# Optimization experiments

Measured on AMD Instinct MI355X. Metric: run time of the kernel, lower is better.

## Reference

```python
import jax, jax.numpy as jnp
import numpy as np

N = 100_000   # nodes
E = 1_000_000 # edges
D_IN = 64
H = 64
G = 64        # graphs in batch
OUT = 2


def gcn_conv(x, edge_index, W, b):
    # PyG GCNConv: add self-loops, symmetric D^-1/2 (A+I) D^-1/2 normalization
    h = x @ W                                   # [N, H]
    src, dst = edge_index[0], edge_index[1]
    n = x.shape[0]
    deg = jax.ops.segment_sum(jnp.ones(E, x.dtype), dst, num_segments=n) + 1.0  # +1 self loop
    dinv = jax.lax.rsqrt(deg)                   # [N]
    norm = dinv[src] * dinv[dst]                # [E]
    msg = h[src] * norm[:, None]                # gather + scale [E, H]
    agg = jax.ops.segment_sum(msg, dst, num_segments=n)
    agg = agg + h * (dinv * dinv)[:, None]      # self-loop term
    return agg + b


def setup_inputs() -> dict:
    key = jax.random.key(0)
    ks = jax.random.split(key, 8)
    x = jax.random.normal(ks[0], (N, D_IN), jnp.float32)
    edge_index = jax.random.randint(ks[1], (2, E), 0, N, dtype=jnp.int64)
    batch = jnp.sort(jax.random.randint(ks[2], (N,), 0, G, dtype=jnp.int64))
    graph_feats = jax.random.normal(ks[3], (G, 1), jnp.float32)
    W1 = jax.random.normal(ks[4], (D_IN, H), jnp.float32) / np.sqrt(D_IN)
    b1 = jnp.zeros((H,), jnp.float32)
    W2 = jax.random.normal(ks[5], (H, H), jnp.float32) / np.sqrt(H)
    b2 = jnp.zeros((H,), jnp.float32)
    Wlin = jax.random.normal(ks[6], (H + 1, OUT), jnp.float32) / np.sqrt(H + 1)
    blin = jnp.zeros((OUT,), jnp.float32)
    return {"x": x, "edge_index": edge_index, "batch": batch,
            "graph_feats": graph_feats, "W1": W1, "b1": b1,
            "W2": W2, "b2": b2, "Wlin": Wlin, "blin": blin}


def reference(x, edge_index, batch, graph_feats, W1, b1, W2, b2, Wlin, blin):
    h = jax.nn.relu(gcn_conv(x, edge_index, W1, b1))
    # dropout is identity in eval mode
    h = jax.nn.relu(gcn_conv(h, edge_index, W2, b2))
    pooled = jax.ops.segment_sum(h, batch, num_segments=G)  # global_add_pool [G, H]
    feats = jnp.concatenate([pooled, graph_feats], axis=1)  # [G, H+1]
    return feats @ Wlin + blin
```

## Files before the change

### kernel.cpp

```cpp
#include <hip/hip_runtime.h>

#define H 64
#define G 64
#define OUT 2
#define MAXBUK 128
#define BSHIFT 10
#define CAP 12288

typedef unsigned int uint32;
using short8 = __attribute__((ext_vector_type(8))) short;
using f32x4  = __attribute__((ext_vector_type(4))) float;

union ABFrag { uint32 u[4]; uint4 q; short8 v; };

__device__ inline float bf16lo(uint32 u) { return __uint_as_float(u << 16); }
__device__ inline float bf16hi(uint32 u) { return __uint_as_float(u & 0xffff0000u); }
__device__ inline uint32 packbf16(float a, float b) {
    uint32 ua = __float_as_uint(a);
    uint32 ub = __float_as_uint(b);
    ua = (ua + 0x7fffu + ((ua >> 16) & 1u)) >> 16;
    ub = (ub + 0x7fffu + ((ub >> 16) & 1u)) & 0xffff0000u;
    return ua | ub;
}

__global__ __launch_bounds__(256) void k_setup(const float* __restrict__ W1,
                                               const float* __restrict__ W2,
                                               uint32* __restrict__ Wb,
                                               float* __restrict__ pooled,
                                               int* __restrict__ bcnt) {
    int blk = blockIdx.x;
    int t = threadIdx.x;
    if (blk < 2) {
        const float* W = blk ? W2 : W1;
        uint32* dw = Wb + blk * 2048;
        for (int i = t; i < 2048; i += 256) {
            int r = i & 3;
            int lane = (i >> 2) & 63;
            int slot = i >> 8;
            int ct = slot >> 1, ks = slot & 1;
            int col = ct * 16 + (lane & 15);
            int k0 = ks * 32 + (lane >> 4) * 8;
            float a = W[(k0 + 2 * r) * 64 + col];
            float b = W[(k0 + 2 * r + 1) * 64 + col];
            dw[i] = packbf16(a, b);
        }
    } else {
        for (int i = t; i < G * H; i += 256) pooled[i] = 0.0f;
        if (t < MAXBUK) bcnt[t] = 0;
    }
}

__global__ __launch_bounds__(256) void k_bhist(const int* __restrict__ dst,
                                               int* __restrict__ bcnt, int e, int nbuk) {
    __shared__ int h[MAXBUK];
    for (int i = threadIdx.x; i < MAXBUK; i += 256) h[i] = 0;
    __syncthreads();
    int stride = gridDim.x * 256;
    for (int i = blockIdx.x * 256 + threadIdx.x; i < e; i += stride)
        atomicAdd(&h[__builtin_nontemporal_load(&dst[i]) >> BSHIFT], 1);
    __syncthreads();
    for (int i = threadIdx.x; i < nbuk; i += 256)
        if (h[i]) atomicAdd(&bcnt[i], h[i]);
}

__global__ void k_bscan(const int* __restrict__ bcnt, int* __restrict__ bbase,
                        int* __restrict__ bcur, int nbuk) {
    if (threadIdx.x == 0) {
        int run = 0;
        for (int i = 0; i < nbuk; ++i) {
            bbase[i] = run; bcur[i] = run; run += bcnt[i];
        }
        bbase[nbuk] = run;
    }
}

__global__ __launch_bounds__(256) void k_bscatter(const int* __restrict__ src,
                                                  const int* __restrict__ dst,
                                                  int* __restrict__ bcur,
                                                  int2* __restrict__ inter, int e) {
    __shared__ int cnt[MAXBUK];
    __shared__ int run[MAXBUK];
    int per = (e + gridDim.x - 1) / gridDim.x;
    int lo = blockIdx.x * per, hi = min(lo + per, e);
    for (int i = threadIdx.x; i < MAXBUK; i += 256) cnt[i] = 0;
    __syncthreads();
    for (int i = lo + threadIdx.x; i < hi; i += 256)
        atomicAdd(&cnt[dst[i] >> BSHIFT], 1);
    __syncthreads();
    if (threadIdx.x < MAXBUK) {
        int c = cnt[threadIdx.x];
        run[threadIdx.x] = c ? atomicAdd(&bcur[threadIdx.x], c) : 0;
        cnt[threadIdx.x] = 0;
    }
    __syncthreads();
    for (int i = lo + threadIdx.x; i < hi; i += 256) {
        int d = dst[i];
        int s = src[i];
        int b = d >> BSHIFT;
        int pos = run[b] + atomicAdd(&cnt[b], 1);
        inter[pos] = make_int2(s, d);
    }
}

__global__ __launch_bounds__(256) void k_build(const int2* __restrict__ inter,
                                               const int* __restrict__ bbase,
                                               int* __restrict__ rowptr,
                                               float* __restrict__ dinv,
                                               int* __restrict__ csr,
                                               int n, int nbuk) {
    __shared__ int cnt[1024];
    __shared__ int scn[1024];
    __shared__ int part[256];
    __shared__ int stage[CAP];
    int b = blockIdx.x;
    int t = threadIdx.x;
    int nlo = b << BSHIFT;
    int nhi = min(nlo + 1024, n);
    int nn = nhi - nlo;
    int e0 = bbase[b], e1 = bbase[b + 1];
    int ne = e1 - e0;
    for (int i = t; i < nn; i += 256) cnt[i] = 0;
    __syncthreads();
    for (int i = t; i < ne; i += 256)
        atomicAdd(&cnt[inter[e0 + i].y - nlo], 1);
    __syncthreads();
    int base4 = 4 * t;
    int sum = 0;
    for (int j = 0; j < 4; ++j) {
        int idx = base4 + j;
        int v = (idx < nn) ? cnt[idx] : 0;
        if (idx < nn) scn[idx] = sum;
        sum += v;
    }
    part[t] = sum;
    __syncthreads();
    for (int off = 1; off < 256; off <<= 1) {
        int v = (t >= off) ? part[t - off] : 0;
        __syncthreads();
        part[t] += v;
        __syncthreads();
    }
    int pbase = (t == 0) ? 0 : part[t - 1];
    for (int j = 0; j < 4; ++j) {
        int idx = base4 + j;
        if (idx < nn) scn[idx] += pbase;
    }
    __syncthreads();
    for (int i = t; i < nn; i += 256) {
        rowptr[nlo + i] = e0 + scn[i];
        dinv[nlo + i] = rsqrtf((float)cnt[i] + 1.0f);
    }
    if (b == 0 && t == 0) rowptr[n] = bbase[nbuk];
    for (int i = t; i < nn; i += 256) cnt[i] = 0;
    __syncthreads();
    for (int i = t; i < ne; i += 256) {
        int2 p = inter[e0 + i];
        int ln = p.y - nlo;
        int pos = scn[ln] + atomicAdd(&cnt[ln], 1);
        if (pos < CAP) stage[pos] = p.x;
        else csr[e0 + pos] = p.x;
    }
    __syncthreads();
    int m = min(ne, CAP);
    for (int i = t; i < m; i += 256) csr[e0 + i] = stage[i];
}

template <int BFIN>
__global__ __launch_bounds__(256) void k_gemm_mfma(const void* __restrict__ Xv,
                                                   const uint32* __restrict__ Wb,
                                                   const float* __restrict__ dinv,
                                                   uint32* __restrict__ Y, int n) {
    int lane = threadIdx.x & 63;
    int wave = threadIdx.x >> 6;
    int l15 = lane & 15;
    int grp = lane >> 4;
    ABFrag bf[4][2];
    const uint4* Wb4 = (const uint4*)Wb;
#pragma unroll
    for (int ct = 0; ct < 4; ++ct)
#pragma unroll
        for (int ks = 0; ks < 2; ++ks)
            bf[ct][ks].q = Wb4[(ct * 2 + ks) * 64 + lane];

    int rbase0 = blockIdx.x * 128 + wave * 32;
    f32x4 acc[2][4] = {};
#pragma unroll
    for (int sub = 0; sub < 2; ++sub) {
        int row = min(rbase0 + sub * 16 + l15, n - 1);
        ABFrag a[2];
        if (BFIN) {
            const uint4* X4 = (const uint4*)Xv;
#pragma unroll
            for (int ks = 0; ks < 2; ++ks)
                a[ks].q = X4[(size_t)row * 8 + ks * 4 + grp];
        } else {
            const float4* X4 = (const float4*)Xv;
#pragma unroll
            for (int ks = 0; ks < 2; ++ks) {
                float4 f0 = X4[(size_t)row * 16 + ks * 8 + grp * 2];
                float4 f1 = X4[(size_t)row * 16 + ks * 8 + grp * 2 + 1];
                a[ks].u[0] = packbf16(f0.x, f0.y);
                a[ks].u[1] = packbf16(f0.z, f0.w);
                a[ks].u[2] = packbf16(f1.x, f1.y);
                a[ks].u[3] = packbf16(f1.z, f1.w);
            }
        }
#pragma unroll
        for (int ct = 0; ct < 4; ++ct) {
            acc[sub][ct] = __builtin_amdgcn_mfma_f32_16x16x32_bf16(a[0].v, bf[ct][0].v,
                                                                   acc[sub][ct], 0, 0, 0);
            acc[sub][ct] = __builtin_amdgcn_mfma_f32_16x16x32_bf16(a[1].v, bf[ct][1].v,
                                                                   acc[sub][ct], 0, 0, 0);
        }
    }
#pragma unroll
    for (int sub = 0; sub < 2; ++sub) {
        int rb = rbase0 + sub * 16;
#pragma unroll
        for (int r = 0; r < 4; ++r) {
            int row = rb + grp * 4 + r;
            float dd = dinv[min(row, n - 1)];
#pragma unroll
            for (int ct = 0; ct < 4; ++ct) {
                float v = acc[sub][ct][r] * dd;
                float w = __shfl_xor(v, 1);
                if (!(lane & 1) && row < n)
                    Y[(size_t)row * 32 + ct * 8 + (l15 >> 1)] = packbf16(v, w);
            }
        }
    }
}

template <int DOPOOL>
__global__ __launch_bounds__(256) void k_aggregate(const uint32* __restrict__ h,
                                                   const int* __restrict__ csrs,
                                                   const int* __restrict__ rowptr,
                                                   const float* __restrict__ dinv,
                                                   const float* __restrict__ b,
                                                   const int* __restrict__ batch,
                                                   uint32* __restrict__ hout,
                                                   float* __restrict__ pooled, int n) {
    __shared__ float red[8][64];
    __shared__ int sg[8];
    int tid = threadIdx.x;
    int wave = tid >> 6;
    int lane = tid & 63;
    int half = lane >> 5;
    int hl = lane & 31;
    int slot = wave * 2 + half;
    int node = blockIdx.x * 8 + slot;
    bool active = node < n;
    float o0 = 0.f, o1 = 0.f;
    if (active) {
        int r0 = rowptr[node];
        int r1 = rowptr[node + 1];
        int m = r1 - 1;
        int mc = max(m, 0);
        uint32 sv = h[(size_t)node * 32 + hl];
        float acc0 = bf16lo(sv);
        float acc1 = bf16hi(sv);
        int s[16];
#pragma unroll
        for (int j = 0; j < 16; ++j)
            s[j] = __builtin_nontemporal_load(&csrs[min(r0 + j, mc)]);
        uint32 g[16];
#pragma unroll
        for (int j = 0; j < 16; ++j)
            g[j] = (r0 + j <= m) ? h[(size_t)s[j] * 32 + hl] : 0u;
#pragma unroll
        for (int j = 0; j < 16; ++j) {
            acc0 += bf16lo(g[j]);
            acc1 += bf16hi(g[j]);
        }
        for (int e = r0 + 16; e < r1; e += 8) {
            int t1 = min(e + 1, m), t2 = min(e + 2, m), t3 = min(e + 3, m);
            int t4 = min(e + 4, m), t5 = min(e + 5, m), t6 = min(e + 6, m);
            int t7 = min(e + 7, m);
            int u0 = csrs[e],  u1 = csrs[t1], u2 = csrs[t2], u3 = csrs[t3];
            int u4 = csrs[t4], u5 = csrs[t5], u6 = csrs[t6], u7 = csrs[t7];
            uint32 q0 = h[(size_t)u0 * 32 + hl];
            uint32 q1 = (e + 1 <= m) ? h[(size_t)u1 * 32 + hl] : 0u;
            uint32 q2 = (e + 2 <= m) ? h[(size_t)u2 * 32 + hl] : 0u;
            uint32 q3 = (e + 3 <= m) ? h[(size_t)u3 * 32 + hl] : 0u;
            uint32 q4 = (e + 4 <= m) ? h[(size_t)u4 * 32 + hl] : 0u;
            uint32 q5 = (e + 5 <= m) ? h[(size_t)u5 * 32 + hl] : 0u;
            uint32 q6 = (e + 6 <= m) ? h[(size_t)u6 * 32 + hl] : 0u;
            uint32 q7 = (e + 7 <= m) ? h[(size_t)u7 * 32 + hl] : 0u;
            acc0 += (bf16lo(q0) + bf16lo(q1)) + (bf16lo(q2) + bf16lo(q3)) +
                    (bf16lo(q4) + bf16lo(q5)) + (bf16lo(q6) + bf16lo(q7));
            acc1 += (bf16hi(q0) + bf16hi(q1)) + (bf16hi(q2) + bf16hi(q3)) +
                    (bf16hi(q4) + bf16hi(q5)) + (bf16hi(q6) + bf16hi(q7));
        }
        float dd = dinv[node];
        o0 = acc0 * dd + b[2 * hl + 0];
        o1 = acc1 * dd + b[2 * hl + 1];
        o0 = o0 > 0.f ? o0 : 0.f;
        o1 = o1 > 0.f ? o1 : 0.f;
        if (!DOPOOL) hout[(size_t)node * 32 + hl] = packbf16(o0, o1);
    }
    if (DOPOOL) {
        red[slot][2 * hl + 0] = active ? o0 : 0.f;
        red[slot][2 * hl + 1] = active ? o1 : 0.f;
        if (hl == 0) sg[slot] = active ? batch[node] : -1;
        __syncthreads();
        if (wave == 0) {
            float s = red[0][lane];
            int gcur = sg[0];
            for (int w = 1; w < 8; ++w) {
                int gw = sg[w];
                if (gw < 0) break;
                if (gw == gcur) {
                    s += red[w][lane];
                } else {
                    if (gcur >= 0) atomicAdd(&pooled[gcur * H + lane], s);
                    s = red[w][lane];
                    gcur = gw;
                }
            }
            if (gcur >= 0) atomicAdd(&pooled[gcur * H + lane], s);
        }
    }
}

__global__ void k_final(const float* __restrict__ pooled, const float* __restrict__ gf,
                        const float* __restrict__ Wlin, const float* __restrict__ blin,
                        float* __restrict__ out) {
    int t = threadIdx.x;
    if (t >= G * OUT) return;
    int g = t >> 1, o = t & 1;
    float acc = blin[o];
#pragma unroll
    for (int j = 0; j < 64; ++j) acc += pooled[g * H + j] * Wlin[j * OUT + o];
    acc += gf[g] * Wlin[64 * OUT + o];
    out[g * OUT + o] = acc;
}

extern "C" void kernel_launch(void* const* d_in, const int* in_sizes, int n_in,
                              void* d_out, int out_size, void* d_ws, size_t ws_size,
                              hipStream_t stream) {
    const float* x          = (const float*)d_in[0];
    const int*   edge_index = (const int*)d_in[1];
    const int*   batch      = (const int*)d_in[2];
    const float* gf         = (const float*)d_in[3];
    const float* W1         = (const float*)d_in[4];
    const float* b1         = (const float*)d_in[5];
    const float* W2         = (const float*)d_in[6];
    const float* b2         = (const float*)d_in[7];
    const float* Wlin       = (const float*)d_in[8];
    const float* blin       = (const float*)d_in[9];
    float* out = (float*)d_out;

    const int N = in_sizes[0] / H;
    const int E = in_sizes[1] / 2;
    const int* src = edge_index;
    const int* dst = edge_index + E;
    const int NBUK = (N + (1 << BSHIFT) - 1) >> BSHIFT;

    float* ws = (float*)d_ws;
    float* dinv   = ws;
    uint32* bufA  = (uint32*)(dinv + N);
    uint32* bufB  = bufA + (size_t)N * 32;
    float* pooled = (float*)(bufB + (size_t)N * 32);
    int*   rowptr = (int*)(pooled + G * H);
    int*   bcnt   = rowptr + (N + 1);
    int*   bbase  = bcnt + MAXBUK;
    int*   bcur   = bbase + (MAXBUK + 1);
    size_t off = (size_t)(bcur + MAXBUK - (int*)d_ws);
    off = (off + 3) & ~(size_t)3;
    uint32* Wb   = (uint32*)d_ws + off;
    int*   csrs  = (int*)(Wb + 2 * 2048);
    size_t off2 = (size_t)(csrs + E - (int*)d_ws);
    off2 = (off2 + 1) & ~(size_t)1;
    int2*  inter = (int2*)((int*)d_ws + off2);

    const int T = 256;

    k_setup<<<3, T, 0, stream>>>(W1, W2, Wb, pooled, bcnt);
    k_bhist<<<256, T, 0, stream>>>(dst, bcnt, E, NBUK);
    k_bscan<<<1, 64, 0, stream>>>(bcnt, bbase, bcur, NBUK);
    k_bscatter<<<128, T, 0, stream>>>(src, dst, bcur, inter, E);
    k_build<<<NBUK, T, 0, stream>>>(inter, bbase, rowptr, dinv, csrs, N, NBUK);

    const int NBG = (N + 127) / 128;

    k_gemm_mfma<0><<<NBG, T, 0, stream>>>(x, Wb, dinv, bufA, N);
    k_aggregate<0><<<(N + 7) / 8, T, 0, stream>>>(bufA, csrs, rowptr, dinv, b1, batch,
                                                  bufB, pooled, N);

    k_gemm_mfma<1><<<NBG, T, 0, stream>>>(bufB, Wb + 2048, dinv, bufA, N);
    k_aggregate<1><<<(N + 7) / 8, T, 0, stream>>>(bufA, csrs, rowptr, dinv, b2, batch,
                                                  nullptr, pooled, N);

    k_final<<<1, 128, 0, stream>>>(pooled, gf, Wlin, blin, out);
}
```

Baseline: 175.6 us.

## Fold bucket scan into histogram, pack edge records, vectorize aggregation gathers

```diff
diff --git a/kernel.cpp b/kernel.cpp
--- a/kernel.cpp
+++ b/kernel.cpp
@@ -27,7 +27,8 @@
                                                const float* __restrict__ W2,
                                                uint32* __restrict__ Wb,
                                                float* __restrict__ pooled,
-                                               int* __restrict__ bcnt) {
+                                               int* __restrict__ bcnt,
+                                               int* __restrict__ done) {
     int blk = blockIdx.x;
     int t = threadIdx.x;
     if (blk < 2) {
@@ -47,37 +48,43 @@
     } else {
         for (int i = t; i < G * H; i += 256) pooled[i] = 0.0f;
         if (t < MAXBUK) bcnt[t] = 0;
+        if (t == 0) *done = 0;
     }
 }
 
 __global__ __launch_bounds__(256) void k_bhist(const int* __restrict__ dst,
-                                               int* __restrict__ bcnt, int e, int nbuk) {
-    __shared__ int h[MAXBUK];
-    for (int i = threadIdx.x; i < MAXBUK; i += 256) h[i] = 0;
+                                               int* __restrict__ bcnt,
+                                               int* __restrict__ bbase,
+                                               int* __restrict__ bcur,
+                                               int* __restrict__ done,
+                                               int e, int nbuk) {
+    __shared__ int hh[MAXBUK];
+    for (int i = threadIdx.x; i < MAXBUK; i += 256) hh[i] = 0;
     __syncthreads();
     int stride = gridDim.x * 256;
     for (int i = blockIdx.x * 256 + threadIdx.x; i < e; i += stride)
-        atomicAdd(&h[__builtin_nontemporal_load(&dst[i]) >> BSHIFT], 1);
+        atomicAdd(&hh[__builtin_nontemporal_load(&dst[i]) >> BSHIFT], 1);
     __syncthreads();
     for (int i = threadIdx.x; i < nbuk; i += 256)
-        if (h[i]) atomicAdd(&bcnt[i], h[i]);
-}
-
-__global__ void k_bscan(const int* __restrict__ bcnt, int* __restrict__ bbase,
-                        int* __restrict__ bcur, int nbuk) {
+        if (hh[i]) atomicAdd(&bcnt[i], hh[i]);
     if (threadIdx.x == 0) {
-        int run = 0;
-        for (int i = 0; i < nbuk; ++i) {
-            bbase[i] = run; bcur[i] = run; run += bcnt[i];
-        }
-        bbase[nbuk] = run;
+        __threadfence();
+        int ticket = atomicAdd(done, 1);
+        if (ticket == (int)gridDim.x - 1) {
+            int run = 0;
+            for (int i = 0; i < nbuk; ++i) {
+                int c = atomicAdd(&bcnt[i], 0);
+                bbase[i] = run; bcur[i] = run; run += c;
+            }
+            bbase[nbuk] = run;
+        }
     }
 }
 
 __global__ __launch_bounds__(256) void k_bscatter(const int* __restrict__ src,
                                                   const int* __restrict__ dst,
                                                   int* __restrict__ bcur,
-                                                  int2* __restrict__ inter, int e) {
+                                                  uint32* __restrict__ inter, int e) {
     __shared__ int cnt[MAXBUK];
     __shared__ int run[MAXBUK];
     int per = (e + gridDim.x - 1) / gridDim.x;
@@ -97,12 +104,13 @@
         int d = dst[i];
         int s = src[i];
         int b = d >> BSHIFT;
+        int ln = d & ((1 << BSHIFT) - 1);
         int pos = run[b] + atomicAdd(&cnt[b], 1);
-        inter[pos] = make_int2(s, d);
-    }
-}
-
-__global__ __launch_bounds__(256) void k_build(const int2* __restrict__ inter,
+        inter[pos] = ((uint32)ln << 17) | (uint32)s;
+    }
+}
+
+__global__ __launch_bounds__(256) void k_build(const uint32* __restrict__ inter,
                                                const int* __restrict__ bbase,
                                                int* __restrict__ rowptr,
                                                float* __restrict__ dinv,
@@ -122,7 +130,7 @@
     for (int i = t; i < nn; i += 256) cnt[i] = 0;
     __syncthreads();
     for (int i = t; i < ne; i += 256)
-        atomicAdd(&cnt[inter[e0 + i].y - nlo], 1);
+        atomicAdd(&cnt[inter[e0 + i] >> 17], 1);
     __syncthreads();
     int base4 = 4 * t;
     int sum = 0;
@@ -154,11 +162,12 @@
     for (int i = t; i < nn; i += 256) cnt[i] = 0;
     __syncthreads();
     for (int i = t; i < ne; i += 256) {
-        int2 p = inter[e0 + i];
-        int ln = p.y - nlo;
+        uint32 p = inter[e0 + i];
+        int ln = p >> 17;
+        int s = p & 0x1FFFF;
         int pos = scn[ln] + atomicAdd(&cnt[ln], 1);
-        if (pos < CAP) stage[pos] = p.x;
-        else csr[e0 + pos] = p.x;
+        if (pos < CAP) stage[pos] = s;
+        else csr[e0 + pos] = s;
     }
     __syncthreads();
     int m = min(ne, CAP);
@@ -247,60 +256,79 @@
     int lane = tid & 63;
     int half = lane >> 5;
     int hl = lane & 31;
+    int grp = hl >> 3;
+    int sub = hl & 7;
     int slot = wave * 2 + half;
     int node = blockIdx.x * 8 + slot;
     bool active = node < n;
-    float o0 = 0.f, o1 = 0.f;
+    const uint4* h4 = (const uint4*)h;
+    float acc[8] = {};
+    float o[8] = {};
     if (active) {
         int r0 = rowptr[node];
         int r1 = rowptr[node + 1];
         int m = r1 - 1;
-        int mc = max(m, 0);
-        uint32 sv = h[(size_t)node * 32 + hl];
-        float acc0 = bf16lo(sv);
-        float acc1 = bf16hi(sv);
-        int s[16];
-#pragma unroll
-        for (int j = 0; j < 16; ++j)
-            s[j] = __builtin_nontemporal_load(&csrs[min(r0 + j, mc)]);
-        uint32 g[16];
-#pragma unroll
-        for (int j = 0; j < 16; ++j)
-            g[j] = (r0 + j <= m) ? h[(size_t)s[j] * 32 + hl] : 0u;
-#pragma unroll
-        for (int j = 0; j < 16; ++j) {
-            acc0 += bf16lo(g[j]);
-            acc1 += bf16hi(g[j]);
-        }
-        for (int e = r0 + 16; e < r1; e += 8) {
-            int t1 = min(e + 1, m), t2 = min(e + 2, m), t3 = min(e + 3, m);
-            int t4 = min(e + 4, m), t5 = min(e + 5, m), t6 = min(e + 6, m);
-            int t7 = min(e + 7, m);
-            int u0 = csrs[e],  u1 = csrs[t1], u2 = csrs[t2], u3 = csrs[t3];
-            int u4 = csrs[t4], u5 = csrs[t5], u6 = csrs[t6], u7 = csrs[t7];
-            uint32 q0 = h[(size_t)u0 * 32 + hl];
-            uint32 q1 = (e + 1 <= m) ? h[(size_t)u1 * 32 + hl] : 0u;
-            uint32 q2 = (e + 2 <= m) ? h[(size_t)u2 * 32 + hl] : 0u;
-            uint32 q3 = (e + 3 <= m) ? h[(size_t)u3 * 32 + hl] : 0u;
-            uint32 q4 = (e + 4 <= m) ? h[(size_t)u4 * 32 + hl] : 0u;
-            uint32 q5 = (e + 5 <= m) ? h[(size_t)u5 * 32 + hl] : 0u;
-            uint32 q6 = (e + 6 <= m) ? h[(size_t)u6 * 32 + hl] : 0u;
-            uint32 q7 = (e + 7 <= m) ? h[(size_t)u7 * 32 + hl] : 0u;
-            acc0 += (bf16lo(q0) + bf16lo(q1)) + (bf16lo(q2) + bf16lo(q3)) +
-                    (bf16lo(q4) + bf16lo(q5)) + (bf16lo(q6) + bf16lo(q7));
-            acc1 += (bf16hi(q0) + bf16hi(q1)) + (bf16hi(q2) + bf16hi(q3)) +
-                    (bf16hi(q4) + bf16hi(q5)) + (bf16hi(q6) + bf16hi(q7));
-        }
+        for (int e = r0; e < r1; e += 16) {
+            int eA = e + grp, eB = e + 4 + grp, eC = e + 8 + grp, eD = e + 12 + grp;
+            int sA = csrs[min(eA, m)];
+            int sB = csrs[min(eB, m)];
+            int sC = csrs[min(eC, m)];
+            int sD = csrs[min(eD, m)];
+            uint4 gA = h4[(size_t)sA * 8 + sub];
+            uint4 gB = h4[(size_t)sB * 8 + sub];
+            uint4 gC = h4[(size_t)sC * 8 + sub];
+            uint4 gD = h4[(size_t)sD * 8 + sub];
+            if (eA > m) { gA.x = gA.y = gA.z = gA.w = 0u; }
+            if (eB > m) { gB.x = gB.y = gB.z = gB.w = 0u; }
+            if (eC > m) { gC.x = gC.y = gC.z = gC.w = 0u; }
+            if (eD > m) { gD.x = gD.y = gD.z = gD.w = 0u; }
+            acc[0] += bf16lo(gA.x) + bf16lo(gB.x) + bf16lo(gC.x) + bf16lo(gD.x);
+            acc[1] += bf16hi(gA.x) + bf16hi(gB.x) + bf16hi(gC.x) + bf16hi(gD.x);
+            acc[2] += bf16lo(gA.y) + bf16lo(gB.y) + bf16lo(gC.y) + bf16lo(gD.y);
+            acc[3] += bf16hi(gA.y) + bf16hi(gB.y) + bf16hi(gC.y) + bf16hi(gD.y);
+            acc[4] += bf16lo(gA.z) + bf16lo(gB.z) + bf16lo(gC.z) + bf16lo(gD.z);
+            acc[5] += bf16hi(gA.z) + bf16hi(gB.z) + bf16hi(gC.z) + bf16hi(gD.z);
+            acc[6] += bf16lo(gA.w) + bf16lo(gB.w) + bf16lo(gC.w) + bf16lo(gD.w);
+            acc[7] += bf16hi(gA.w) + bf16hi(gB.w) + bf16hi(gC.w) + bf16hi(gD.w);
+        }
+#pragma unroll
+        for (int c = 0; c < 8; ++c) {
+            acc[c] += __shfl_xor(acc[c], 8);
+            acc[c] += __shfl_xor(acc[c], 16);
+        }
+        uint4 sv = h4[(size_t)node * 8 + sub];
         float dd = dinv[node];
-        o0 = acc0 * dd + b[2 * hl + 0];
-        o1 = acc1 * dd + b[2 * hl + 1];
-        o0 = o0 > 0.f ? o0 : 0.f;
-        o1 = o1 > 0.f ? o1 : 0.f;
-        if (!DOPOOL) hout[(size_t)node * 32 + hl] = packbf16(o0, o1);
+        if (grp == 0) {
+            float s0 = bf16lo(sv.x), s1 = bf16hi(sv.x);
+            float s2 = bf16lo(sv.y), s3 = bf16hi(sv.y);
+            float s4 = bf16lo(sv.z), s5 = bf16hi(sv.z);
+            float s6 = bf16lo(sv.w), s7 = bf16hi(sv.w);
+            o[0] = (acc[0] + s0) * dd + b[hl * 8 + 0];
+            o[1] = (acc[1] + s1) * dd + b[hl * 8 + 1];
+            o[2] = (acc[2] + s2) * dd + b[hl * 8 + 2];
+            o[3] = (acc[3] + s3) * dd + b[hl * 8 + 3];
+            o[4] = (acc[4] + s4) * dd + b[hl * 8 + 4];
+            o[5] = (acc[5] + s5) * dd + b[hl * 8 + 5];
+            o[6] = (acc[6] + s6) * dd + b[hl * 8 + 6];
+            o[7] = (acc[7] + s7) * dd + b[hl * 8 + 7];
+#pragma unroll
+            for (int c = 0; c < 8; ++c) o[c] = o[c] > 0.f ? o[c] : 0.f;
+            if (!DOPOOL) {
+                uint4 u;
+                u.x = packbf16(o[0], o[1]);
+                u.y = packbf16(o[2], o[3]);
+                u.z = packbf16(o[4], o[5]);
+                u.w = packbf16(o[6], o[7]);
+                ((uint4*)hout)[(size_t)node * 8 + hl] = u;
+            }
+        }
     }
     if (DOPOOL) {
-        red[slot][2 * hl + 0] = active ? o0 : 0.f;
-        red[slot][2 * hl + 1] = active ? o1 : 0.f;
+        if (grp == 0) {
+#pragma unroll
+            for (int c = 0; c < 8; ++c)
+                red[slot][hl * 8 + c] = active ? o[c] : 0.f;
+        }
         if (hl == 0) sg[slot] = active ? batch[node] : -1;
         __syncthreads();
         if (wave == 0) {
@@ -365,19 +393,17 @@
     int*   bcnt   = rowptr + (N + 1);
     int*   bbase  = bcnt + MAXBUK;
     int*   bcur   = bbase + (MAXBUK + 1);
-    size_t off = (size_t)(bcur + MAXBUK - (int*)d_ws);
+    int*   done   = bcur + MAXBUK;
+    size_t off = (size_t)(done + 1 - (int*)d_ws);
     off = (off + 3) & ~(size_t)3;
     uint32* Wb   = (uint32*)d_ws + off;
     int*   csrs  = (int*)(Wb + 2 * 2048);
-    size_t off2 = (size_t)(csrs + E - (int*)d_ws);
-    off2 = (off2 + 1) & ~(size_t)1;
-    int2*  inter = (int2*)((int*)d_ws + off2);
+    uint32* inter = (uint32*)(csrs + E);
 
     const int T = 256;
 
-    k_setup<<<3, T, 0, stream>>>(W1, W2, Wb, pooled, bcnt);
-    k_bhist<<<256, T, 0, stream>>>(dst, bcnt, E, NBUK);
-    k_bscan<<<1, 64, 0, stream>>>(bcnt, bbase, bcur, NBUK);
+    k_setup<<<3, T, 0, stream>>>(W1, W2, Wb, pooled, bcnt, done);
+    k_bhist<<<256, T, 0, stream>>>(dst, bcnt, bbase, bcur, done, E, NBUK);
     k_bscatter<<<128, T, 0, stream>>>(src, dst, bcur, inter, E);
     k_build<<<NBUK, T, 0, stream>>>(inter, bbase, rowptr, dinv, csrs, N, NBUK);
 
```

Measured after the change: 169.7 us (median of 2 runs). -3.4%, faster.
